# Kernel optimization log

Measured on AMD Instinct MI355X. Metric: run time of the kernel, lower is better.

The kernel has to match this reference:

```python
import jax, jax.numpy as jnp
import numpy as np

N = 262144      # total nodes (B subgraphs of S nodes)
S = 32          # nodes per enclosing subgraph
B = N // S      # number of (user,item) subgraphs = 8192
E = 4194304     # total edges (avg degree 16)


def setup_inputs() -> dict:
    key = jax.random.key(0)
    ks = jax.random.split(key, 8)
    # structural labels per subgraph: node0=user-root(0), 1..15 user-neighbors(1),
    # node16=item-root(2), 17..31 item-neighbors(3)
    pat = np.full(S, 3, dtype=np.int32)
    pat[0] = 0
    pat[1:16] = 1
    pat[16] = 2
    labels = jnp.asarray(np.tile(pat, B))
    feats = jax.nn.one_hot(labels, 4, dtype=jnp.float32)  # [N,4]
    # block-local random edges (edges never cross subgraph boundaries)
    blk = jax.random.randint(ks[0], (E,), 0, B) * S
    row = blk + jax.random.randint(ks[1], (E,), 0, S)
    col = blk + jax.random.randint(ks[2], (E,), 0, S)
    def kaiming(k, fi, fo):
        return jax.random.normal(k, (fi, fo), jnp.float32) * np.sqrt(2.0 / fi)
    return {
        'feats': feats,
        'row': row.astype(jnp.int32), 'col': col.astype(jnp.int32),
        'W1': kaiming(ks[3], 4, 32),  'b1': jnp.zeros((32,), jnp.float32),
        'W2': kaiming(ks[4], 32, 32), 'b2': jnp.zeros((32,), jnp.float32),
        'W3': kaiming(ks[5], 32, 32), 'b3': jnp.zeros((32,), jnp.float32),
        'lin1_W': kaiming(ks[6], 192, 32), 'lin1_b': jnp.zeros((32,), jnp.float32),
        'lin2_W': kaiming(ks[7], 32, 1),   'lin2_b': jnp.zeros((1,), jnp.float32),
    }


def reference(feats, row, col, W1, b1, W2, b2, W3, b3, lin1_W, lin1_b, lin2_W, lin2_b):
    n = feats.shape[0]
    ones = jnp.ones(row.shape, feats.dtype)
    # DGL GraphConv norm='both': D_out^{-1/2} on src side, D_in^{-1/2} on dst side,
    # degrees clamped to min 1 (allow_zero_in_degree=True)
    out_deg = jnp.maximum(jax.ops.segment_sum(ones, row, num_segments=n), 1.0)
    in_deg = jnp.maximum(jax.ops.segment_sum(ones, col, num_segments=n), 1.0)
    norm_s = jax.lax.rsqrt(out_deg)  # [N]
    norm_d = jax.lax.rsqrt(in_deg)   # [N]

    def gconv(x, W, b):
        msg = x[row] * norm_s[row, None]                       # gather [E,d]
        agg = jax.ops.segment_sum(msg, col, num_segments=n)    # scatter [N,d]
        return jnp.tanh((agg * norm_d[:, None]) @ W + b)

    x = feats
    reps = []
    for W, b in ((W1, b1), (W2, b2), (W3, b3)):
        x = gconv(x, W, b)
        reps.append(x)
    all_rep = jnp.concatenate(reps, axis=1)  # [N, 96] JK-concat

    # root-node selection: exactly B user roots and B item roots by construction
    u_idx = jnp.nonzero(feats[:, 0] == 1.0, size=B)[0]
    i_idx = jnp.nonzero(feats[:, 2] == 1.0, size=B)[0]
    h = jnp.concatenate([all_rep[u_idx], all_rep[i_idx]], axis=1)  # [B,192]
    h = jax.nn.relu(h @ lin1_W + lin1_b)
    # eval mode: F.dropout(training=False) is identity
    return (h @ lin2_W + lin2_b).squeeze(-1)  # [B]
```

## Files before the change

### kernel.cpp

```cpp
#include <hip/hip_runtime.h>

typedef __attribute__((ext_vector_type(8))) short bf16x8;
typedef __attribute__((ext_vector_type(16))) float f32x16;
typedef unsigned int u32;
typedef unsigned short u16;

#define GA   1024
#define NBKT 128
#define BATCH 4096
#define CAPC 128
#define NCPY 4

union BF8 { bf16x8 v; u16 u[8]; u32 w[4]; };

static __device__ __forceinline__ u16 f2bf(float f) {
    u32 u = __float_as_uint(f);
    return (u16)((u + 0x7FFFu + ((u >> 16) & 1u)) >> 16);
}
static __device__ __forceinline__ u32 f2bf2(float lo, float hi) {
    u32 r;
    asm("v_cvt_pk_bf16_f32 %0, %1, %2" : "=v"(r) : "v"(lo), "v"(hi));
    return r;
}
static __device__ __forceinline__ float tanh_fast(float x) {
    float xc = fminf(fmaxf(x, -15.f), 15.f);
    float t = __expf(2.f * xc);
    return (t - 1.f) * __builtin_amdgcn_rcpf(t + 1.f);
}

__global__ __launch_bounds__(256) void scatterA(
    const int* __restrict__ row, const int* __restrict__ col,
    u32* __restrict__ count, u16* __restrict__ ebuf, int E, int CH)
{
    __shared__ u32 bcnt[NBKT], bpos[NBKT];
    __shared__ u32 stage[BATCH];
    __shared__ u32 w0s;
    const int t = threadIdx.x, g = blockIdx.x;

    const int beg = g * CH, end = min(E, beg + CH);
    const int nE = end - beg;
    const int4* r4 = reinterpret_cast<const int4*>(row + beg);
    const int4* c4 = reinterpret_cast<const int4*>(col + beg);

    if (t < NBKT) bcnt[t] = 0;
    __syncthreads();

    u32 code[16];
    int rank[16];
    #pragma unroll
    for (int kv = 0; kv < 4; ++kv) {
        int i4 = kv * 256 + t;
        bool v = (i4 * 4) < nE;
        int4 r = v ? r4[i4] : make_int4(0, 0, 0, 0);
        int4 c = v ? c4[i4] : make_int4(0, 0, 0, 0);
        int k0 = kv * 4;
        code[k0 + 0] = v ? (u32)(((r.x >> 5) << 10) | ((r.x & 31) << 5) | (c.x & 31)) : ~0u;
        code[k0 + 1] = v ? (u32)(((r.y >> 5) << 10) | ((r.y & 31) << 5) | (c.y & 31)) : ~0u;
        code[k0 + 2] = v ? (u32)(((r.z >> 5) << 10) | ((r.z & 31) << 5) | (c.z & 31)) : ~0u;
        code[k0 + 3] = v ? (u32)(((r.w >> 5) << 10) | ((r.w & 31) << 5) | (c.w & 31)) : ~0u;
    }
    #pragma unroll
    for (int k = 0; k < 16; ++k)
        rank[k] = (code[k] != ~0u) ? (int)atomicAdd(&bcnt[code[k] >> 16], 1u) : 0;
    __syncthreads();

    u32 v_ = (t < NBKT) ? bcnt[t] : 0;
    u32 s = v_;
    #pragma unroll
    for (int off = 1; off < 64; off <<= 1) {
        u32 u_ = __shfl_up(s, off, 64);
        if ((t & 63) >= off) s += u_;
    }
    if (t == 63) w0s = s;
    __syncthreads();
    if (t < NBKT) {
        bpos[t] = s - v_ + ((t >= 64) ? w0s : 0);
        count[g * NBKT + t] = (v_ > CAPC) ? (u32)CAPC : v_;
    }
    __syncthreads();

    #pragma unroll
    for (int k = 0; k < 16; ++k)
        if (code[k] != ~0u) stage[bpos[code[k] >> 16] + rank[k]] = code[k];
    __syncthreads();

    for (int j = t; j < nE; j += 256) {
        u32 cv = stage[j];
        u32 b = cv >> 16;
        u32 idx = (u32)j - bpos[b];
        if (idx < CAPC)
            ebuf[(b << 17) + ((u32)g << 7) + idx] = (u16)cv;
    }
}

__global__ __launch_bounds__(1024) void countB(
    const u16* __restrict__ ebuf, const u32* __restrict__ count, u32* __restrict__ adj)
{
    __shared__ u32 nib[8192];
    const int t = threadIdx.x, w = blockIdx.x;
    const int bucket = w >> 2;
    const int g0h = (w & 3) * 256;

    #pragma unroll
    for (int i = t; i < 8192; i += 1024) nib[i] = 0;
    __syncthreads();

    const int wave = t >> 6, lane = t & 63;
    const int g0 = g0h + wave * 16;
    u32 mycnt = (lane < 16) ? count[(g0 + lane) * NBKT + bucket] : 0;
    const u32 base = ((u32)bucket << 17);

    #pragma unroll 4
    for (int it = 0; it < 16; ++it) {
        u32 cnt = (u32)__shfl((int)mycnt, it, 64);
        u32 sb = base + ((u32)(g0 + it) << 7);
        u32 lc = ebuf[sb + lane];
        if ((u32)lane < cnt)
            atomicAdd(&nib[lc >> 3], 1u << ((lc & 7) << 2));
        if (cnt > 64) {
            for (u32 i = 64 + (u32)lane; i < cnt; i += 64) {
                u32 lc2 = ebuf[sb + i];
                atomicAdd(&nib[lc2 >> 3], 1u << ((lc2 & 7) << 2));
            }
        }
    }
    __syncthreads();
    u32* dst = adj + (size_t)w * 8192;
    #pragma unroll
    for (int i = t; i < 8192; i += 1024) dst[i] = nib[i];
}

__global__ __launch_bounds__(256, 4) void igmc_kernel(
    const float4* __restrict__ feats4,
    const u32* __restrict__ adj, int NB,
    const float* __restrict__ W1, const float* __restrict__ B1,
    const float* __restrict__ W2, const float* __restrict__ B2,
    const float* __restrict__ W3, const float* __restrict__ B3,
    const float* __restrict__ lin1W, const float* __restrict__ lin1b,
    const float* __restrict__ lin2W, const float* __restrict__ lin2b,
    float* __restrict__ out)
{
    __shared__ u32 raw[4][128];
    __shared__ __align__(16) u16 Tb[4][2][32 * 36];
    __shared__ float nsL[4][32];
    __shared__ __align__(16) float4 fst[4][32];
    __shared__ float repL[4][192];

    const int tid = threadIdx.x;
    const int w = tid >> 6, l = tid & 63, h = l >> 5, c = l & 31;
    const int b = blockIdx.x * 4 + w;
    const bool valid = (b < NB);

    if (valid) {
        const u32* a0 = adj + (size_t)(b >> 6) * (8192 * NCPY) + (size_t)(b & 63) * 128;
        uint2 r0 = *reinterpret_cast<const uint2*>(a0 + 2 * l);
        uint2 r1 = *reinterpret_cast<const uint2*>(a0 + 8192 + 2 * l);
        uint2 r2 = *reinterpret_cast<const uint2*>(a0 + 16384 + 2 * l);
        uint2 r3 = *reinterpret_cast<const uint2*>(a0 + 24576 + 2 * l);
        uint2 rw;
        rw.x = r0.x + r1.x + r2.x + r3.x;
        rw.y = r0.y + r1.y + r2.y + r3.y;
        *reinterpret_cast<uint2*>(&raw[w][2 * l]) = rw;
        if (h == 0) fst[w][c] = feats4[(size_t)b * 32 + c];
    }
    __syncthreads();

    float cf[16];
    int colsum = 0;
    #pragma unroll
    for (int f = 0; f < 2; ++f)
        #pragma unroll
        for (int i = 0; i < 8; ++i) {
            int u = 16 * f + 8 * h + i;
            u32 word = raw[w][u * 4 + (c >> 3)];
            int v = (word >> ((c & 7) << 2)) & 15;
            cf[f * 8 + i] = (float)v;
            colsum += v;
        }
    colsum += __shfl_xor(colsum, 32, 64);
    const float ndr = rsqrtf(fmaxf((float)colsum, 1.f));

    if (h == 0) {
        u32 r0 = raw[w][4 * c], r1 = raw[w][4 * c + 1];
        u32 r2 = raw[w][4 * c + 2], r3 = raw[w][4 * c + 3];
        const u32 m = 0x0F0F0F0Fu;
        u32 bs = (r0 & m) + ((r0 >> 4) & m) + (r1 & m) + ((r1 >> 4) & m)
               + (r2 & m) + ((r2 >> 4) & m) + (r3 & m) + ((r3 >> 4) & m);
        u32 p2 = (bs & 0x00FF00FFu) + ((bs >> 8) & 0x00FF00FFu);
        u32 s = (p2 + (p2 >> 16)) & 0xFFFFu;
        nsL[w][c] = rsqrtf(fmaxf((float)s, 1.f));
    }
    __syncthreads();

    BF8 Mf[2];
    #pragma unroll
    for (int f = 0; f < 2; ++f)
        #pragma unroll
        for (int j = 0; j < 4; ++j) {
            int u0 = 16 * f + 8 * h + 2 * j;
            Mf[f].w[j] = f2bf2(cf[f * 8 + 2 * j]     * nsL[w][u0]     * ndr,
                               cf[f * 8 + 2 * j + 1] * nsL[w][u0 + 1] * ndr);
        }

    float w1r0 = W1[c], w1r1 = W1[32 + c], w1r2 = W1[64 + c], w1r3 = W1[96 + c];
    const float b1r = B1[c], b2r = B2[c], b3r = B3[c];
    BF8 W2f[2], W3f[2];
    #pragma unroll
    for (int f = 0; f < 2; ++f)
        #pragma unroll
        for (int j = 0; j < 4; ++j) {
            int k0 = 16 * f + 8 * h + 2 * j;
            W2f[f].w[j] = f2bf2(W2[k0 * 32 + c], W2[(k0 + 1) * 32 + c]);
            W3f[f].w[j] = f2bf2(W3[k0 * 32 + c], W3[(k0 + 1) * 32 + c]);
        }

    BF8 Xa, Xb;
    #pragma unroll
    for (int f = 0; f < 2; ++f)
        #pragma unroll
        for (int j = 0; j < 4; ++j) {
            int u0 = 16 * f + 8 * h + 2 * j;
            float4 x0 = fst[w][u0];
            float4 x1 = fst[w][u0 + 1];
            u32 pk = f2bf2(x0.x * w1r0 + x0.y * w1r1 + x0.z * w1r2 + x0.w * w1r3,
                           x1.x * w1r0 + x1.y * w1r1 + x1.z * w1r2 + x1.w * w1r3);
            if (f == 0) Xa.w[j] = pk; else Xb.w[j] = pk;
        }

    f32x16 acc;
    float th[16];
    u32 p[8], q[8];

    auto zero_acc = [&]() {
        #pragma unroll
        for (int j = 0; j < 16; ++j) acc[j] = 0.f;
    };
    auto pack_exchange = [&](BF8& Ra, BF8& Rb) {
        #pragma unroll
        for (int j = 0; j < 8; ++j) p[j] = f2bf2(th[2 * j], th[2 * j + 1]);
        #pragma unroll
        for (int j = 0; j < 8; ++j) q[j] = __shfl_xor((int)p[j], 32, 64);
        Ra.w[0] = h ? q[2] : p[0];  Ra.w[1] = h ? q[3] : p[1];
        Ra.w[2] = h ? p[2] : q[0];  Ra.w[3] = h ? p[3] : q[1];
        Rb.w[0] = h ? q[6] : p[4];  Rb.w[1] = h ? q[7] : p[5];
        Rb.w[2] = h ? p[6] : q[4];  Rb.w[3] = h ? p[7] : q[5];
    };

    zero_acc();
    acc = __builtin_amdgcn_mfma_f32_32x32x16_bf16(Mf[0].v, Xa.v, acc, 0, 0, 0);
    acc = __builtin_amdgcn_mfma_f32_32x32x16_bf16(Mf[1].v, Xb.v, acc, 0, 0, 0);
    #pragma unroll
    for (int j = 0; j < 16; ++j) th[j] = tanh_fast(acc[j] + b1r);
    if (h == 0) { repL[w][c] = th[0]; repL[w][96 + c] = th[8]; }
    pack_exchange(Xa, Xb);

    zero_acc();
    acc = __builtin_amdgcn_mfma_f32_32x32x16_bf16(Mf[0].v, Xa.v, acc, 0, 0, 0);
    acc = __builtin_amdgcn_mfma_f32_32x32x16_bf16(Mf[1].v, Xb.v, acc, 0, 0, 0);
    #pragma unroll
    for (int j = 0; j < 16; ++j) {
        int r = (j & 3) + 8 * (j >> 2) + 4 * h;
        Tb[w][0][r * 36 + c] = f2bf(acc[j]);
    }
    __syncthreads();
    {
        const u32* t32 = reinterpret_cast<const u32*>(&Tb[w][0][0]);
        int base = 18 * c + 4 * h;
        Xa.w[0] = t32[base];     Xa.w[1] = t32[base + 1];
        Xa.w[2] = t32[base + 2]; Xa.w[3] = t32[base + 3];
        Xb.w[0] = t32[base + 8]; Xb.w[1] = t32[base + 9];
        Xb.w[2] = t32[base + 10]; Xb.w[3] = t32[base + 11];
    }
    zero_acc();
    acc = __builtin_amdgcn_mfma_f32_32x32x16_bf16(Xa.v, W2f[0].v, acc, 0, 0, 0);
    acc = __builtin_amdgcn_mfma_f32_32x32x16_bf16(Xb.v, W2f[1].v, acc, 0, 0, 0);
    #pragma unroll
    for (int j = 0; j < 16; ++j) th[j] = tanh_fast(acc[j] + b2r);
    if (h == 0) { repL[w][32 + c] = th[0]; repL[w][128 + c] = th[8]; }
    pack_exchange(Xa, Xb);

    zero_acc();
    acc = __builtin_amdgcn_mfma_f32_32x32x16_bf16(Mf[0].v, Xa.v, acc, 0, 0, 0);
    acc = __builtin_amdgcn_mfma_f32_32x32x16_bf16(Mf[1].v, Xb.v, acc, 0, 0, 0);
    #pragma unroll
    for (int j = 0; j < 16; ++j) {
        int r = (j & 3) + 8 * (j >> 2) + 4 * h;
        Tb[w][1][r * 36 + c] = f2bf(acc[j]);
    }
    __syncthreads();
    {
        const u32* t32 = reinterpret_cast<const u32*>(&Tb[w][1][0]);
        int base = 18 * c + 4 * h;
        Xa.w[0] = t32[base];     Xa.w[1] = t32[base + 1];
        Xa.w[2] = t32[base + 2]; Xa.w[3] = t32[base + 3];
        Xb.w[0] = t32[base + 8]; Xb.w[1] = t32[base + 9];
        Xb.w[2] = t32[base + 10]; Xb.w[3] = t32[base + 11];
    }
    zero_acc();
    acc = __builtin_amdgcn_mfma_f32_32x32x16_bf16(Xa.v, W3f[0].v, acc, 0, 0, 0);
    acc = __builtin_amdgcn_mfma_f32_32x32x16_bf16(Xb.v, W3f[1].v, acc, 0, 0, 0);
    if (h == 0) {
        repL[w][64 + c]  = tanh_fast(acc[0] + b3r);
        repL[w][160 + c] = tanh_fast(acc[8] + b3r);
    }
    __syncthreads();

    {
        float a = 0.f;
        #pragma unroll 8
        for (int k2 = 0; k2 < 96; ++k2) {
            int k = h * 96 + k2;
            a += repL[w][k] * lin1W[k * 32 + c];
        }
        a += __shfl_xor(a, 32, 64);
        a += lin1b[c];
        float hr = fmaxf(a, 0.f);
        float pp = hr * lin2W[c];
        #pragma unroll
        for (int off = 16; off > 0; off >>= 1) pp += __shfl_xor(pp, off, 64);
        if (l == 0 && valid) out[b] = pp + lin2b[0];
    }
}

__global__ __launch_bounds__(256) void build_adj(
    const int* __restrict__ row, const int* __restrict__ col,
    u32* __restrict__ adj, int E)
{
    const int gid = blockIdx.x * blockDim.x + threadIdx.x;
    const int stride = gridDim.x * blockDim.x;
    for (int e = gid; e < E; e += stride) {
        int r = row[e], c = col[e];
        int blk = r >> 5;
        int nibidx = ((r & 31) << 5) | (c & 31);
        size_t addr = (size_t)(blk >> 6) * (8192 * NCPY) + (size_t)(blk & 63) * 128 + (nibidx >> 3);
        atomicAdd(&adj[addr], 1u << ((nibidx & 7) << 2));
    }
}

extern "C" void kernel_launch(void* const* d_in, const int* in_sizes, int n_in,
                              void* d_out, int out_size, void* d_ws, size_t ws_size,
                              hipStream_t stream)
{
    const float* feats = (const float*)d_in[0];
    const int*   row   = (const int*)d_in[1];
    const int*   col   = (const int*)d_in[2];
    const float* W1    = (const float*)d_in[3];
    const float* b1    = (const float*)d_in[4];
    const float* W2    = (const float*)d_in[5];
    const float* b2    = (const float*)d_in[6];
    const float* W3    = (const float*)d_in[7];
    const float* b3    = (const float*)d_in[8];
    const float* lin1W = (const float*)d_in[9];
    const float* lin1b = (const float*)d_in[10];
    const float* lin2W = (const float*)d_in[11];
    const float* lin2b = (const float*)d_in[12];

    const int N = in_sizes[0] / 4;
    const int E = in_sizes[1];
    const int NB = N / 32;

    const int CH = BATCH;
    const size_t off_ebuf = (size_t)GA * NBKT * 4;
    const size_t off_adj  = off_ebuf + (size_t)NBKT * GA * CAPC * 2;
    const size_t adj_bytes = (size_t)NCPY * NBKT * 8192 * 4;
    const size_t need     = off_adj + adj_bytes;
    const bool fast = (ws_size >= need) && (NB == 8192) && ((E & 3) == 0)
                      && ((size_t)E <= (size_t)GA * BATCH);

    if (fast) {
        u32* count = (u32*)d_ws;
        u16* ebuf  = (u16*)((char*)d_ws + off_ebuf);
        u32* adj   = (u32*)((char*)d_ws + off_adj);
        scatterA<<<GA, 256, 0, stream>>>(row, col, count, ebuf, E, CH);
        countB<<<NCPY * NBKT, 1024, 0, stream>>>(ebuf, count, adj);
        igmc_kernel<<<NB / 4, 256, 0, stream>>>(
            reinterpret_cast<const float4*>(feats), adj, NB,
            W1, b1, W2, b2, W3, b3, lin1W, lin1b, lin2W, lin2b,
            (float*)d_out);
    } else {
        u32* adj = (u32*)d_ws;
        hipMemsetAsync(d_ws, 0, (size_t)NCPY * ((NB + 63) / 64) * 8192 * 4, stream);
        int eblocks = (E + 255) / 256;
        if (eblocks > 2048) eblocks = 2048;
        build_adj<<<eblocks, 256, 0, stream>>>(row, col, adj, E);
        igmc_kernel<<<(NB + 3) / 4, 256, 0, stream>>>(
            reinterpret_cast<const float4*>(feats), adj, NB,
            W1, b1, W2, b2, W3, b3, lin1W, lin1b, lin2W, lin2b,
            (float*)d_out);
    }
}
```

Measured before the change: 49.71 us.

## Fuse adjacency counting into GNN kernel with finer 512-bucket scatter

Scatter now uses 512 buckets of 16 subgraphs each, with per-segment capacity 32 and byte counts. The separate countB kernel and the global adjacency buffer go away: each 512-thread block of the fused kernel builds its bucket's nibble adjacency in shared memory, then runs the GCN/MLP for 16 subgraphs in two passes of 8 waves. This removes one launch and a global round trip for the adjacency. In exchange the fused kernel has only 512 blocks and must do the counting phase before any compute, and CAPC=32 could truncate segments that have more edges than that.

```diff
diff --git a/kernel.cpp b/kernel.cpp
--- a/kernel.cpp
+++ b/kernel.cpp
@@ -4,12 +4,12 @@
 typedef __attribute__((ext_vector_type(16))) float f32x16;
 typedef unsigned int u32;
 typedef unsigned short u16;
-
-#define GA   1024
-#define NBKT 128
+typedef unsigned char u8;
+
+#define GA    1024
+#define NBKT  512
 #define BATCH 4096
-#define CAPC 128
-#define NCPY 4
+#define CAPC  32
 
 union BF8 { bf16x8 v; u16 u[8]; u32 w[4]; };
 
@@ -30,11 +30,11 @@
 
 __global__ __launch_bounds__(256) void scatterA(
     const int* __restrict__ row, const int* __restrict__ col,
-    u32* __restrict__ count, u16* __restrict__ ebuf, int E, int CH)
+    u8* __restrict__ cnt8, u16* __restrict__ ebuf, int E, int CH)
 {
     __shared__ u32 bcnt[NBKT], bpos[NBKT];
     __shared__ u32 stage[BATCH];
-    __shared__ u32 w0s;
+    __shared__ u32 wsum[4];
     const int t = threadIdx.x, g = blockIdx.x;
 
     const int beg = g * CH, end = min(E, beg + CH);
@@ -42,7 +42,7 @@
     const int4* r4 = reinterpret_cast<const int4*>(row + beg);
     const int4* c4 = reinterpret_cast<const int4*>(col + beg);
 
-    if (t < NBKT) bcnt[t] = 0;
+    bcnt[t] = 0; bcnt[t + 256] = 0;
     __syncthreads();
 
     u32 code[16];
@@ -61,78 +61,49 @@
     }
     #pragma unroll
     for (int k = 0; k < 16; ++k)
-        rank[k] = (code[k] != ~0u) ? (int)atomicAdd(&bcnt[code[k] >> 16], 1u) : 0;
-    __syncthreads();
-
-    u32 v_ = (t < NBKT) ? bcnt[t] : 0;
-    u32 s = v_;
+        rank[k] = (code[k] != ~0u) ? (int)atomicAdd(&bcnt[code[k] >> 14], 1u) : 0;
+    __syncthreads();
+
+    const u32 a0 = bcnt[2 * t], a1 = bcnt[2 * t + 1];
+    const u32 s2 = a0 + a1;
+    u32 inc = s2;
     #pragma unroll
     for (int off = 1; off < 64; off <<= 1) {
-        u32 u_ = __shfl_up(s, off, 64);
-        if ((t & 63) >= off) s += u_;
-    }
-    if (t == 63) w0s = s;
-    __syncthreads();
-    if (t < NBKT) {
-        bpos[t] = s - v_ + ((t >= 64) ? w0s : 0);
-        count[g * NBKT + t] = (v_ > CAPC) ? (u32)CAPC : v_;
+        u32 u_ = __shfl_up(inc, off, 64);
+        if ((t & 63) >= off) inc += u_;
+    }
+    if ((t & 63) == 63) wsum[t >> 6] = inc;
+    __syncthreads();
+    u32 woff = 0;
+    for (int wv = 0; wv < (t >> 6); ++wv) woff += wsum[wv];
+    const u32 excl = woff + inc - s2;
+    bpos[2 * t] = excl;
+    bpos[2 * t + 1] = excl + a0;
+    {
+        u32 c0 = a0 > CAPC ? (u32)CAPC : a0;
+        u32 c1 = a1 > CAPC ? (u32)CAPC : a1;
+        *reinterpret_cast<u16*>(&cnt8[(size_t)g * NBKT + 2 * t]) = (u16)(c0 | (c1 << 8));
     }
     __syncthreads();
 
     #pragma unroll
     for (int k = 0; k < 16; ++k)
-        if (code[k] != ~0u) stage[bpos[code[k] >> 16] + rank[k]] = code[k];
+        if (code[k] != ~0u) stage[bpos[code[k] >> 14] + rank[k]] = code[k];
     __syncthreads();
 
     for (int j = t; j < nE; j += 256) {
         u32 cv = stage[j];
-        u32 b = cv >> 16;
+        u32 b = cv >> 14;
         u32 idx = (u32)j - bpos[b];
         if (idx < CAPC)
-            ebuf[(b << 17) + ((u32)g << 7) + idx] = (u16)cv;
-    }
-}
-
-__global__ __launch_bounds__(1024) void countB(
-    const u16* __restrict__ ebuf, const u32* __restrict__ count, u32* __restrict__ adj)
-{
-    __shared__ u32 nib[8192];
-    const int t = threadIdx.x, w = blockIdx.x;
-    const int bucket = w >> 2;
-    const int g0h = (w & 3) * 256;
-
-    #pragma unroll
-    for (int i = t; i < 8192; i += 1024) nib[i] = 0;
-    __syncthreads();
-
-    const int wave = t >> 6, lane = t & 63;
-    const int g0 = g0h + wave * 16;
-    u32 mycnt = (lane < 16) ? count[(g0 + lane) * NBKT + bucket] : 0;
-    const u32 base = ((u32)bucket << 17);
-
-    #pragma unroll 4
-    for (int it = 0; it < 16; ++it) {
-        u32 cnt = (u32)__shfl((int)mycnt, it, 64);
-        u32 sb = base + ((u32)(g0 + it) << 7);
-        u32 lc = ebuf[sb + lane];
-        if ((u32)lane < cnt)
-            atomicAdd(&nib[lc >> 3], 1u << ((lc & 7) << 2));
-        if (cnt > 64) {
-            for (u32 i = 64 + (u32)lane; i < cnt; i += 64) {
-                u32 lc2 = ebuf[sb + i];
-                atomicAdd(&nib[lc2 >> 3], 1u << ((lc2 & 7) << 2));
-            }
-        }
-    }
-    __syncthreads();
-    u32* dst = adj + (size_t)w * 8192;
-    #pragma unroll
-    for (int i = t; i < 8192; i += 1024) dst[i] = nib[i];
-}
-
-__global__ __launch_bounds__(256, 4) void igmc_kernel(
+            ebuf[((size_t)b << 15) + ((u32)g << 5) + idx] = (u16)(cv & 0x3FFF);
+    }
+}
+
+__global__ __launch_bounds__(512, 4) void igmc_fused(
     const float4* __restrict__ feats4,
-    const u32* __restrict__ adj, int NB,
+    const u16* __restrict__ ebuf, const u8* __restrict__ cnt8,
+    const u32* __restrict__ adj_fb, int NB,
     const float* __restrict__ W1, const float* __restrict__ B1,
     const float* __restrict__ W2, const float* __restrict__ B2,
     const float* __restrict__ W3, const float* __restrict__ B3,
@@ -140,69 +111,45 @@
     const float* __restrict__ lin2W, const float* __restrict__ lin2b,
     float* __restrict__ out)
 {
-    __shared__ u32 raw[4][128];
-    __shared__ __align__(16) u16 Tb[4][2][32 * 36];
-    __shared__ float nsL[4][32];
-    __shared__ __align__(16) float4 fst[4][32];
-    __shared__ float repL[4][192];
-
-    const int tid = threadIdx.x;
-    const int w = tid >> 6, l = tid & 63, h = l >> 5, c = l & 31;
-    const int b = blockIdx.x * 4 + w;
-    const bool valid = (b < NB);
-
-    if (valid) {
-        const u32* a0 = adj + (size_t)(b >> 6) * (8192 * NCPY) + (size_t)(b & 63) * 128;
-        uint2 r0 = *reinterpret_cast<const uint2*>(a0 + 2 * l);
-        uint2 r1 = *reinterpret_cast<const uint2*>(a0 + 8192 + 2 * l);
-        uint2 r2 = *reinterpret_cast<const uint2*>(a0 + 16384 + 2 * l);
-        uint2 r3 = *reinterpret_cast<const uint2*>(a0 + 24576 + 2 * l);
-        uint2 rw;
-        rw.x = r0.x + r1.x + r2.x + r3.x;
-        rw.y = r0.y + r1.y + r2.y + r3.y;
-        *reinterpret_cast<uint2*>(&raw[w][2 * l]) = rw;
-        if (h == 0) fst[w][c] = feats4[(size_t)b * 32 + c];
-    }
-    __syncthreads();
-
-    float cf[16];
-    int colsum = 0;
-    #pragma unroll
-    for (int f = 0; f < 2; ++f)
-        #pragma unroll
-        for (int i = 0; i < 8; ++i) {
-            int u = 16 * f + 8 * h + i;
-            u32 word = raw[w][u * 4 + (c >> 3)];
-            int v = (word >> ((c & 7) << 2)) & 15;
-            cf[f * 8 + i] = (float)v;
-            colsum += v;
-        }
-    colsum += __shfl_xor(colsum, 32, 64);
-    const float ndr = rsqrtf(fmaxf((float)colsum, 1.f));
-
-    if (h == 0) {
-        u32 r0 = raw[w][4 * c], r1 = raw[w][4 * c + 1];
-        u32 r2 = raw[w][4 * c + 2], r3 = raw[w][4 * c + 3];
-        const u32 m = 0x0F0F0F0Fu;
-        u32 bs = (r0 & m) + ((r0 >> 4) & m) + (r1 & m) + ((r1 >> 4) & m)
-               + (r2 & m) + ((r2 >> 4) & m) + (r3 & m) + ((r3 >> 4) & m);
-        u32 p2 = (bs & 0x00FF00FFu) + ((bs >> 8) & 0x00FF00FFu);
-        u32 s = (p2 + (p2 >> 16)) & 0xFFFFu;
-        nsL[w][c] = rsqrtf(fmaxf((float)s, 1.f));
-    }
-    __syncthreads();
-
-    BF8 Mf[2];
-    #pragma unroll
-    for (int f = 0; f < 2; ++f)
-        #pragma unroll
-        for (int j = 0; j < 4; ++j) {
-            int u0 = 16 * f + 8 * h + 2 * j;
-            Mf[f].w[j] = f2bf2(cf[f * 8 + 2 * j]     * nsL[w][u0]     * ndr,
-                               cf[f * 8 + 2 * j + 1] * nsL[w][u0 + 1] * ndr);
-        }
-
-    float w1r0 = W1[c], w1r1 = W1[32 + c], w1r2 = W1[64 + c], w1r3 = W1[96 + c];
+    __shared__ u32 nib[2048];
+    __shared__ __align__(16) u16 Tb[8][2][32 * 36];
+    __shared__ float nsL[8][32];
+    __shared__ __align__(16) float4 fst[8][32];
+    __shared__ float repL[8][192];
+
+    const int t = threadIdx.x;
+    const int wv = t >> 6, lane = t & 63, h = lane >> 5, c = lane & 31;
+    const int bucket = blockIdx.x;
+
+    for (int i = t; i < 2048; i += 512) nib[i] = 0;
+    __syncthreads();
+    if (ebuf) {
+        const int cbase = wv * 128;
+        u32 my0 = cnt8[(size_t)(cbase + lane) * NBKT + bucket];
+        u32 my1 = cnt8[(size_t)(cbase + 64 + lane) * NBKT + bucket];
+        const u16* src = ebuf + ((size_t)bucket << 15) + (size_t)cbase * CAPC;
+        const int s_ = lane >> 5;
+        #pragma unroll 4
+        for (int i = 0; i < 32; ++i) {
+            u32 cnt = (u32)__shfl((int)my0, 2 * i + s_, 64);
+            u32 lc = src[64 * i + lane];
+            if ((u32)(lane & 31) < cnt)
+                atomicAdd(&nib[lc >> 3], 1u << ((lc & 7) << 2));
+        }
+        const u16* src2 = src + 64 * 32;
+        #pragma unroll 4
+        for (int i = 0; i < 32; ++i) {
+            u32 cnt = (u32)__shfl((int)my1, 2 * i + s_, 64);
+            u32 lc = src2[64 * i + lane];
+            if ((u32)(lane & 31) < cnt)
+                atomicAdd(&nib[lc >> 3], 1u << ((lc & 7) << 2));
+        }
+    } else {
+        for (int i = t; i < 2048; i += 512) nib[i] = adj_fb[(size_t)bucket * 2048 + i];
+    }
+    __syncthreads();
+
+    const float w1r0 = W1[c], w1r1 = W1[32 + c], w1r2 = W1[64 + c], w1r3 = W1[96 + c];
     const float b1r = B1[c], b2r = B2[c], b3r = B3[c];
     BF8 W2f[2], W3f[2];
     #pragma unroll
@@ -214,111 +161,158 @@
             W3f[f].w[j] = f2bf2(W3[k0 * 32 + c], W3[(k0 + 1) * 32 + c]);
         }
 
-    BF8 Xa, Xb;
-    #pragma unroll
-    for (int f = 0; f < 2; ++f)
-        #pragma unroll
-        for (int j = 0; j < 4; ++j) {
-            int u0 = 16 * f + 8 * h + 2 * j;
-            float4 x0 = fst[w][u0];
-            float4 x1 = fst[w][u0 + 1];
-            u32 pk = f2bf2(x0.x * w1r0 + x0.y * w1r1 + x0.z * w1r2 + x0.w * w1r3,
-                           x1.x * w1r0 + x1.y * w1r1 + x1.z * w1r2 + x1.w * w1r3);
-            if (f == 0) Xa.w[j] = pk; else Xb.w[j] = pk;
-        }
-
-    f32x16 acc;
-    float th[16];
-    u32 p[8], q[8];
-
-    auto zero_acc = [&]() {
-        #pragma unroll
-        for (int j = 0; j < 16; ++j) acc[j] = 0.f;
-    };
-    auto pack_exchange = [&](BF8& Ra, BF8& Rb) {
-        #pragma unroll
-        for (int j = 0; j < 8; ++j) p[j] = f2bf2(th[2 * j], th[2 * j + 1]);
-        #pragma unroll
-        for (int j = 0; j < 8; ++j) q[j] = __shfl_xor((int)p[j], 32, 64);
-        Ra.w[0] = h ? q[2] : p[0];  Ra.w[1] = h ? q[3] : p[1];
-        Ra.w[2] = h ? p[2] : q[0];  Ra.w[3] = h ? p[3] : q[1];
-        Rb.w[0] = h ? q[6] : p[4];  Rb.w[1] = h ? q[7] : p[5];
-        Rb.w[2] = h ? p[6] : q[4];  Rb.w[3] = h ? p[7] : q[5];
-    };
-
-    zero_acc();
-    acc = __builtin_amdgcn_mfma_f32_32x32x16_bf16(Mf[0].v, Xa.v, acc, 0, 0, 0);
-    acc = __builtin_amdgcn_mfma_f32_32x32x16_bf16(Mf[1].v, Xb.v, acc, 0, 0, 0);
-    #pragma unroll
-    for (int j = 0; j < 16; ++j) th[j] = tanh_fast(acc[j] + b1r);
-    if (h == 0) { repL[w][c] = th[0]; repL[w][96 + c] = th[8]; }
-    pack_exchange(Xa, Xb);
-
-    zero_acc();
-    acc = __builtin_amdgcn_mfma_f32_32x32x16_bf16(Mf[0].v, Xa.v, acc, 0, 0, 0);
-    acc = __builtin_amdgcn_mfma_f32_32x32x16_bf16(Mf[1].v, Xb.v, acc, 0, 0, 0);
-    #pragma unroll
-    for (int j = 0; j < 16; ++j) {
-        int r = (j & 3) + 8 * (j >> 2) + 4 * h;
-        Tb[w][0][r * 36 + c] = f2bf(acc[j]);
-    }
-    __syncthreads();
-    {
-        const u32* t32 = reinterpret_cast<const u32*>(&Tb[w][0][0]);
-        int base = 18 * c + 4 * h;
-        Xa.w[0] = t32[base];     Xa.w[1] = t32[base + 1];
-        Xa.w[2] = t32[base + 2]; Xa.w[3] = t32[base + 3];
-        Xb.w[0] = t32[base + 8]; Xb.w[1] = t32[base + 9];
-        Xb.w[2] = t32[base + 10]; Xb.w[3] = t32[base + 11];
-    }
-    zero_acc();
-    acc = __builtin_amdgcn_mfma_f32_32x32x16_bf16(Xa.v, W2f[0].v, acc, 0, 0, 0);
-    acc = __builtin_amdgcn_mfma_f32_32x32x16_bf16(Xb.v, W2f[1].v, acc, 0, 0, 0);
-    #pragma unroll
-    for (int j = 0; j < 16; ++j) th[j] = tanh_fast(acc[j] + b2r);
-    if (h == 0) { repL[w][32 + c] = th[0]; repL[w][128 + c] = th[8]; }
-    pack_exchange(Xa, Xb);
-
-    zero_acc();
-    acc = __builtin_amdgcn_mfma_f32_32x32x16_bf16(Mf[0].v, Xa.v, acc, 0, 0, 0);
-    acc = __builtin_amdgcn_mfma_f32_32x32x16_bf16(Mf[1].v, Xb.v, acc, 0, 0, 0);
-    #pragma unroll
-    for (int j = 0; j < 16; ++j) {
-        int r = (j & 3) + 8 * (j >> 2) + 4 * h;
-        Tb[w][1][r * 36 + c] = f2bf(acc[j]);
-    }
-    __syncthreads();
-    {
-        const u32* t32 = reinterpret_cast<const u32*>(&Tb[w][1][0]);
-        int base = 18 * c + 4 * h;
-        Xa.w[0] = t32[base];     Xa.w[1] = t32[base + 1];
-        Xa.w[2] = t32[base + 2]; Xa.w[3] = t32[base + 3];
-        Xb.w[0] = t32[base + 8]; Xb.w[1] = t32[base + 9];
-        Xb.w[2] = t32[base + 10]; Xb.w[3] = t32[base + 11];
-    }
-    zero_acc();
-    acc = __builtin_amdgcn_mfma_f32_32x32x16_bf16(Xa.v, W3f[0].v, acc, 0, 0, 0);
-    acc = __builtin_amdgcn_mfma_f32_32x32x16_bf16(Xb.v, W3f[1].v, acc, 0, 0, 0);
-    if (h == 0) {
-        repL[w][64 + c]  = tanh_fast(acc[0] + b3r);
-        repL[w][160 + c] = tanh_fast(acc[8] + b3r);
-    }
-    __syncthreads();
-
-    {
-        float a = 0.f;
-        #pragma unroll 8
-        for (int k2 = 0; k2 < 96; ++k2) {
-            int k = h * 96 + k2;
-            a += repL[w][k] * lin1W[k * 32 + c];
-        }
-        a += __shfl_xor(a, 32, 64);
-        a += lin1b[c];
-        float hr = fmaxf(a, 0.f);
-        float pp = hr * lin2W[c];
-        #pragma unroll
-        for (int off = 16; off > 0; off >>= 1) pp += __shfl_xor(pp, off, 64);
-        if (l == 0 && valid) out[b] = pp + lin2b[0];
+    for (int it2 = 0; it2 < 2; ++it2) {
+        const int sg = it2 * 8 + wv;
+        const int b = bucket * 16 + sg;
+        const bool valid = (b < NB);
+        const u32* rawp = &nib[sg * 128];
+
+        if (valid && h == 0) fst[wv][c] = feats4[(size_t)b * 32 + c];
+
+        float cf[16];
+        int colsum = 0;
+        #pragma unroll
+        for (int f = 0; f < 2; ++f)
+            #pragma unroll
+            for (int i = 0; i < 8; ++i) {
+                int u = 16 * f + 8 * h + i;
+                u32 word = rawp[u * 4 + (c >> 3)];
+                int v = (word >> ((c & 7) << 2)) & 15;
+                cf[f * 8 + i] = (float)v;
+                colsum += v;
+            }
+        colsum += __shfl_xor(colsum, 32, 64);
+        const float ndr = rsqrtf(fmaxf((float)colsum, 1.f));
+
+        if (h == 0) {
+            u32 r0 = rawp[4 * c], r1 = rawp[4 * c + 1];
+            u32 r2 = rawp[4 * c + 2], r3 = rawp[4 * c + 3];
+            const u32 m = 0x0F0F0F0Fu;
+            u32 bs = (r0 & m) + ((r0 >> 4) & m) + (r1 & m) + ((r1 >> 4) & m)
+                   + (r2 & m) + ((r2 >> 4) & m) + (r3 & m) + ((r3 >> 4) & m);
+            u32 p2 = (bs & 0x00FF00FFu) + ((bs >> 8) & 0x00FF00FFu);
+            u32 s = (p2 + (p2 >> 16)) & 0xFFFFu;
+            nsL[wv][c] = rsqrtf(fmaxf((float)s, 1.f));
+        }
+        __syncthreads();
+
+        BF8 Mf[2];
+        #pragma unroll
+        for (int f = 0; f < 2; ++f)
+            #pragma unroll
+            for (int j = 0; j < 4; ++j) {
+                int u0 = 16 * f + 8 * h + 2 * j;
+                Mf[f].w[j] = f2bf2(cf[f * 8 + 2 * j]     * nsL[wv][u0]     * ndr,
+                                   cf[f * 8 + 2 * j + 1] * nsL[wv][u0 + 1] * ndr);
+            }
+
+        BF8 Xa, Xb;
+        #pragma unroll
+        for (int f = 0; f < 2; ++f)
+            #pragma unroll
+            for (int j = 0; j < 4; ++j) {
+                int u0 = 16 * f + 8 * h + 2 * j;
+                float4 x0 = fst[wv][u0];
+                float4 x1 = fst[wv][u0 + 1];
+                u32 pk = f2bf2(x0.x * w1r0 + x0.y * w1r1 + x0.z * w1r2 + x0.w * w1r3,
+                               x1.x * w1r0 + x1.y * w1r1 + x1.z * w1r2 + x1.w * w1r3);
+                if (f == 0) Xa.w[j] = pk; else Xb.w[j] = pk;
+            }
+
+        f32x16 acc;
+        float th[16];
+        u32 p[8], q[8];
+
+        auto zero_acc = [&]() {
+            #pragma unroll
+            for (int j = 0; j < 16; ++j) acc[j] = 0.f;
+        };
+        auto pack_exchange = [&](BF8& Ra, BF8& Rb) {
+            #pragma unroll
+            for (int j = 0; j < 8; ++j) p[j] = f2bf2(th[2 * j], th[2 * j + 1]);
+            #pragma unroll
+            for (int j = 0; j < 8; ++j) q[j] = __shfl_xor((int)p[j], 32, 64);
+            Ra.w[0] = h ? q[2] : p[0];  Ra.w[1] = h ? q[3] : p[1];
+            Ra.w[2] = h ? p[2] : q[0];  Ra.w[3] = h ? p[3] : q[1];
+            Rb.w[0] = h ? q[6] : p[4];  Rb.w[1] = h ? q[7] : p[5];
+            Rb.w[2] = h ? p[6] : q[4];  Rb.w[3] = h ? p[7] : q[5];
+        };
+
+        zero_acc();
+        acc = __builtin_amdgcn_mfma_f32_32x32x16_bf16(Mf[0].v, Xa.v, acc, 0, 0, 0);
+        acc = __builtin_amdgcn_mfma_f32_32x32x16_bf16(Mf[1].v, Xb.v, acc, 0, 0, 0);
+        #pragma unroll
+        for (int j = 0; j < 16; ++j) th[j] = tanh_fast(acc[j] + b1r);
+        if (h == 0) { repL[wv][c] = th[0]; repL[wv][96 + c] = th[8]; }
+        pack_exchange(Xa, Xb);
+
+        zero_acc();
+        acc = __builtin_amdgcn_mfma_f32_32x32x16_bf16(Mf[0].v, Xa.v, acc, 0, 0, 0);
+        acc = __builtin_amdgcn_mfma_f32_32x32x16_bf16(Mf[1].v, Xb.v, acc, 0, 0, 0);
+        #pragma unroll
+        for (int j = 0; j < 16; ++j) {
+            int r = (j & 3) + 8 * (j >> 2) + 4 * h;
+            Tb[wv][0][r * 36 + c] = f2bf(acc[j]);
+        }
+        __syncthreads();
+        {
+            const u32* t32 = reinterpret_cast<const u32*>(&Tb[wv][0][0]);
+            int base = 18 * c + 4 * h;
+            Xa.w[0] = t32[base];      Xa.w[1] = t32[base + 1];
+            Xa.w[2] = t32[base + 2];  Xa.w[3] = t32[base + 3];
+            Xb.w[0] = t32[base + 8];  Xb.w[1] = t32[base + 9];
+            Xb.w[2] = t32[base + 10]; Xb.w[3] = t32[base + 11];
+        }
+        zero_acc();
+        acc = __builtin_amdgcn_mfma_f32_32x32x16_bf16(Xa.v, W2f[0].v, acc, 0, 0, 0);
+        acc = __builtin_amdgcn_mfma_f32_32x32x16_bf16(Xb.v, W2f[1].v, acc, 0, 0, 0);
+        #pragma unroll
+        for (int j = 0; j < 16; ++j) th[j] = tanh_fast(acc[j] + b2r);
+        if (h == 0) { repL[wv][32 + c] = th[0]; repL[wv][128 + c] = th[8]; }
+        pack_exchange(Xa, Xb);
+
+        zero_acc();
+        acc = __builtin_amdgcn_mfma_f32_32x32x16_bf16(Mf[0].v, Xa.v, acc, 0, 0, 0);
+        acc = __builtin_amdgcn_mfma_f32_32x32x16_bf16(Mf[1].v, Xb.v, acc, 0, 0, 0);
+        #pragma unroll
+        for (int j = 0; j < 16; ++j) {
+            int r = (j & 3) + 8 * (j >> 2) + 4 * h;
+            Tb[wv][1][r * 36 + c] = f2bf(acc[j]);
+        }
+        __syncthreads();
+        {
+            const u32* t32 = reinterpret_cast<const u32*>(&Tb[wv][1][0]);
+            int base = 18 * c + 4 * h;
+            Xa.w[0] = t32[base];      Xa.w[1] = t32[base + 1];
+            Xa.w[2] = t32[base + 2];  Xa.w[3] = t32[base + 3];
+            Xb.w[0] = t32[base + 8];  Xb.w[1] = t32[base + 9];
+            Xb.w[2] = t32[base + 10]; Xb.w[3] = t32[base + 11];
+        }
+        zero_acc();
+        acc = __builtin_amdgcn_mfma_f32_32x32x16_bf16(Xa.v, W3f[0].v, acc, 0, 0, 0);
+        acc = __builtin_amdgcn_mfma_f32_32x32x16_bf16(Xb.v, W3f[1].v, acc, 0, 0, 0);
+        if (h == 0) {
+            repL[wv][64 + c]  = tanh_fast(acc[0] + b3r);
+            repL[wv][160 + c] = tanh_fast(acc[8] + b3r);
+        }
+        __syncthreads();
+
+        {
+            float a = 0.f;
+            #pragma unroll 8
+            for (int k2 = 0; k2 < 96; ++k2) {
+                int k = h * 96 + k2;
+                a += repL[wv][k] * lin1W[k * 32 + c];
+            }
+            a += __shfl_xor(a, 32, 64);
+            a += lin1b[c];
+            float hr = fmaxf(a, 0.f);
+            float pp = hr * lin2W[c];
+            #pragma unroll
+            for (int off = 16; off > 0; off >>= 1) pp += __shfl_xor(pp, off, 64);
+            if (lane == 0 && valid) out[b] = pp + lin2b[0];
+        }
+        __syncthreads();
     }
 }
 
@@ -332,8 +326,7 @@
         int r = row[e], c = col[e];
         int blk = r >> 5;
         int nibidx = ((r & 31) << 5) | (c & 31);
-        size_t addr = (size_t)(blk >> 6) * (8192 * NCPY) + (size_t)(blk & 63) * 128 + (nibidx >> 3);
-        atomicAdd(&adj[addr], 1u << ((nibidx & 7) << 2));
+        atomicAdd(&adj[(size_t)blk * 128 + (nibidx >> 3)], 1u << ((nibidx & 7) << 2));
     }
 }
 
@@ -360,31 +353,29 @@
     const int NB = N / 32;
 
     const int CH = BATCH;
-    const size_t off_ebuf = (size_t)GA * NBKT * 4;
-    const size_t off_adj  = off_ebuf + (size_t)NBKT * GA * CAPC * 2;
-    const size_t adj_bytes = (size_t)NCPY * NBKT * 8192 * 4;
-    const size_t need     = off_adj + adj_bytes;
+    const size_t off_ebuf = (size_t)GA * NBKT;
+    const size_t ebuf_bytes = (size_t)NBKT * GA * CAPC * 2;
+    const size_t need = off_ebuf + ebuf_bytes;
     const bool fast = (ws_size >= need) && (NB == 8192) && ((E & 3) == 0)
                       && ((size_t)E <= (size_t)GA * BATCH);
 
     if (fast) {
-        u32* count = (u32*)d_ws;
-        u16* ebuf  = (u16*)((char*)d_ws + off_ebuf);
-        u32* adj   = (u32*)((char*)d_ws + off_adj);
-        scatterA<<<GA, 256, 0, stream>>>(row, col, count, ebuf, E, CH);
-        countB<<<NCPY * NBKT, 1024, 0, stream>>>(ebuf, count, adj);
-        igmc_kernel<<<NB / 4, 256, 0, stream>>>(
-            reinterpret_cast<const float4*>(feats), adj, NB,
+        u8*  cnt8 = (u8*)d_ws;
+        u16* ebuf = (u16*)((char*)d_ws + off_ebuf);
+        scatterA<<<GA, 256, 0, stream>>>(row, col, cnt8, ebuf, E, CH);
+        igmc_fused<<<NBKT, 512, 0, stream>>>(
+            reinterpret_cast<const float4*>(feats), ebuf, cnt8, nullptr, NB,
             W1, b1, W2, b2, W3, b3, lin1W, lin1b, lin2W, lin2b,
             (float*)d_out);
     } else {
         u32* adj = (u32*)d_ws;
-        hipMemsetAsync(d_ws, 0, (size_t)NCPY * ((NB + 63) / 64) * 8192 * 4, stream);
+        const int nbkt_fb = (NB + 15) / 16;
+        hipMemsetAsync(d_ws, 0, (size_t)nbkt_fb * 2048 * 4, stream);
         int eblocks = (E + 255) / 256;
         if (eblocks > 2048) eblocks = 2048;
         build_adj<<<eblocks, 256, 0, stream>>>(row, col, adj, E);
-        igmc_kernel<<<(NB + 3) / 4, 256, 0, stream>>>(
-            reinterpret_cast<const float4*>(feats), adj, NB,
+        igmc_fused<<<nbkt_fb, 512, 0, stream>>>(
+            reinterpret_cast<const float4*>(feats), nullptr, nullptr, adj, NB,
             W1, b1, W2, b2, W3, b3, lin1W, lin1b, lin2W, lin2b,
             (float*)d_out);
     }
```

New measurement: 65.39 us. +31.5%, slower.
